# Kernel optimization log

Measured on AMD Instinct MI355X. Metric: run time of the kernel, lower is better.

Reference implementation:

```python
import jax, jax.numpy as jnp
import numpy as np

HUGE = jnp.float32(1e31)   # ops.HUGE_INT
EPS = 1e-20
B, AN = 1024, 256
D = 256            # emb_dim
HD = 512           # history_dim
AD = 2 * D         # action_dim
NE, NR = 100000, 400


def setup_inputs() -> dict:
    key = jax.random.key(0)
    ks = jax.random.split(key, 12)
    e = jax.random.randint(ks[0], (B,), 0, NE)
    q = jax.random.randint(ks[1], (B,), 0, NR)
    hstate = jax.random.normal(ks[2], (B, HD), dtype=jnp.float32)
    r_space = jax.random.randint(ks[3], (B, AN), 0, NR)
    e_space = jax.random.randint(ks[4], (B, AN), 0, NE)
    # binary action mask; guarantee at least one valid action per row
    action_mask = (jax.random.uniform(ks[5], (B, AN)) > 0.2).astype(jnp.float32)
    action_mask = action_mask.at[:, 0].set(1.0)
    entity_emb = jax.random.normal(ks[6], (NE, D), dtype=jnp.float32) * 0.02
    relation_emb = jax.random.normal(ks[7], (NR, D), dtype=jnp.float32) * 0.02
    W1 = jax.random.normal(ks[8], (2 * D + HD, AD), dtype=jnp.float32) * (1.0 / np.sqrt(2 * D + HD))
    b1 = jnp.zeros((AD,), dtype=jnp.float32)
    W2 = jax.random.normal(ks[9], (AD, AD), dtype=jnp.float32) * (1.0 / np.sqrt(AD))
    b2 = jnp.zeros((AD,), dtype=jnp.float32)
    return {"e": e, "q": q, "hstate": hstate, "r_space": r_space,
            "e_space": e_space, "action_mask": action_mask,
            "entity_emb": entity_emb, "relation_emb": relation_emb,
            "W1": W1, "b1": b1, "W2": W2, "b2": b2}


def reference(e, q, hstate, r_space, e_space, action_mask,
              entity_emb, relation_emb, W1, b1, W2, b2):
    Q = relation_emb[q]                       # [B, D]
    E = entity_emb[e]                         # [B, D]
    X = jnp.concatenate([E, hstate, Q], axis=-1)          # [B, 2D+HD]
    X = jax.nn.relu(X @ W1 + b1)                          # [B, AD]
    X2 = X @ W2 + b2                                      # [B, AD]
    # action embeddings: [rel_emb[r]; ent_emb[e]] per padded action slot
    A = jnp.concatenate([relation_emb[r_space], entity_emb[e_space]], axis=-1)  # [B, AN, AD]
    scores = jnp.einsum('bad,bd->ba', A, X2) - (1.0 - action_mask) * HUGE      # [B, AN]
    action_dist = jax.nn.softmax(scores, axis=-1)
    entropy = -jnp.sum(action_dist * jnp.log(jnp.clip(action_dist, EPS)), axis=-1)  # [B]
    return action_dist, entropy
```

## Files before the change

### kernel.cpp

```cpp
#include <hip/hip_runtime.h>
#include <math.h>

#define NB   1024
#define NACT 256
#define DIM  256
#define HDIM 512
#define ADIM 512
#define KTOT 1024
#define NE   100000
#define NR   400

typedef __attribute__((ext_vector_type(8))) short bf16x8;
typedef __attribute__((ext_vector_type(4))) float f32x4;

__device__ __forceinline__ unsigned short f2bf(float f) {
    unsigned int u = __float_as_uint(f);
    u += 0x7FFF + ((u >> 16) & 1);
    return (unsigned short)(u >> 16);
}
__device__ __forceinline__ float bf2f(unsigned short u) {
    return __uint_as_float(((unsigned int)u) << 16);
}

__global__ __launch_bounds__(256) void prep_stream(
    const float* __restrict__ ent, const float* __restrict__ rel,
    const float* __restrict__ hstate,
    const int* __restrict__ e, const int* __restrict__ q,
    ushort* __restrict__ entbf, ushort* __restrict__ relbf,
    ushort* __restrict__ Xbf)
{
    const int blk = blockIdx.x, tid = threadIdx.x;
    if (blk < 1024) {
        const float4* src = (const float4*)ent;
        ushort4* dst = (ushort4*)entbf;
        const int start = blk * 6250;
        for (int j = start + tid; j < start + 6250; j += 256) {
            const float4 v = src[j];
            ushort4 o = {f2bf(v.x), f2bf(v.y), f2bf(v.z), f2bf(v.w)};
            dst[j] = o;
        }
    } else if (blk < 1028) {
        const float4* src = (const float4*)rel;
        ushort4* dst = (ushort4*)relbf;
        const int start = (blk - 1024) * 6400;
        for (int j = start + tid; j < start + 6400; j += 256) {
            const float4 v = src[j];
            ushort4 o = {f2bf(v.x), f2bf(v.y), f2bf(v.z), f2bf(v.w)};
            dst[j] = o;
        }
    } else {
        const int b0 = (blk - 1028) * 16;
        const int c = tid * 4;
        for (int r = 0; r < 16; ++r) {
            const int b = b0 + r;
            float4 v;
            if (c < DIM)             v = *(const float4*)(ent + (size_t)e[b] * DIM + c);
            else if (c < DIM + HDIM) v = *(const float4*)(hstate + (size_t)b * HDIM + (c - DIM));
            else                     v = *(const float4*)(rel + (size_t)q[b] * DIM + (c - DIM - HDIM));
            ushort4 o = {f2bf(v.x), f2bf(v.y), f2bf(v.z), f2bf(v.w)};
            *(ushort4*)(Xbf + (size_t)b * KTOT + c) = o;
        }
    }
}

__global__ __launch_bounds__(256) void prep_transpose(
    const float* __restrict__ W1, const float* __restrict__ W2,
    ushort* __restrict__ W1T, ushort* __restrict__ W2T)
{
    __shared__ float t[64][68];
    const int z = blockIdx.z;
    if (z && blockIdx.x >= 8) return;
    const int Kd = z ? 512 : 1024;
    const float* in = z ? W2 : W1;
    ushort* out = z ? W2T : W1T;
    const int k0 = blockIdx.x * 64, n0 = blockIdx.y * 64;
    const int tid = threadIdx.x;
    const int kr = tid >> 2, c = tid & 3;
    #pragma unroll
    for (int j = 0; j < 4; ++j) {
        const float4 v = *(const float4*)(in + (size_t)(k0 + kr) * ADIM + n0 + c * 16 + j * 4);
        *(float4*)&t[kr][c * 16 + j * 4] = v;
    }
    __syncthreads();
    const int nr = tid >> 2;
    ushort tmp[16];
    #pragma unroll
    for (int kk = 0; kk < 16; ++kk) tmp[kk] = f2bf(t[c * 16 + kk][nr]);
    *(uint4*)(out + (size_t)(n0 + nr) * Kd + k0 + c * 16)     = *(uint4*)&tmp[0];
    *(uint4*)(out + (size_t)(n0 + nr) * Kd + k0 + c * 16 + 8) = *(uint4*)&tmp[8];
}

template<int K, bool RELU_BF16>
__global__ __launch_bounds__(256) void gemm_mfma(
    const ushort* __restrict__ A, const ushort* __restrict__ Bt,
    const float* __restrict__ bias, ushort* __restrict__ Cbf,
    float* __restrict__ Cf, int ldc)
{
    __shared__ __align__(16) ushort Als[64][40];
    __shared__ __align__(16) ushort Bls[64][40];
    const int tid  = threadIdx.x;
    const int n0   = blockIdx.x * 64;
    const int m0   = blockIdx.y * 64;
    const int wave = tid >> 6, lane = tid & 63;
    const int q    = lane >> 4, l15 = lane & 15;
    const int sm   = tid >> 2, sc = tid & 3;

    const uint4* ga = (const uint4*)(A  + (size_t)(m0 + sm) * K) + sc;
    const uint4* gb = (const uint4*)(Bt + (size_t)(n0 + sm) * K) + sc;

    f32x4 acc[4];
    #pragma unroll
    for (int mt = 0; mt < 4; ++mt) acc[mt] = (f32x4){0.f, 0.f, 0.f, 0.f};

    uint4 pa = ga[0], pb = gb[0];
    for (int it = 0; it < K / 32; ++it) {
        *(uint4*)&Als[sm][sc * 8] = pa;
        *(uint4*)&Bls[sm][sc * 8] = pb;
        __syncthreads();
        if (it + 1 < K / 32) {
            pa = ga[(it + 1) * 4];
            pb = gb[(it + 1) * 4];
        }
        const bf16x8 bfrag = *(const bf16x8*)&Bls[wave * 16 + l15][q * 8];
        #pragma unroll
        for (int mt = 0; mt < 4; ++mt) {
            const bf16x8 afrag = *(const bf16x8*)&Als[mt * 16 + l15][q * 8];
            acc[mt] = __builtin_amdgcn_mfma_f32_16x16x32_bf16(afrag, bfrag, acc[mt], 0, 0, 0);
        }
        __syncthreads();
    }
    const int n = n0 + wave * 16 + l15;
    const float bv = bias[n];
    #pragma unroll
    for (int mt = 0; mt < 4; ++mt) {
        #pragma unroll
        for (int r = 0; r < 4; ++r) {
            const int m = m0 + mt * 16 + q * 4 + r;
            const float v = acc[mt][r] + bv;
            if (RELU_BF16) Cbf[(size_t)m * ldc + n] = f2bf(fmaxf(v, 0.0f));
            else           Cf [(size_t)m * ldc + n] = v;
        }
    }
}

__global__ __launch_bounds__(512) void scores_kernel(
    const int* __restrict__ r_space, const int* __restrict__ e_space,
    const float* __restrict__ amask,
    const ushort* __restrict__ relbf, const ushort* __restrict__ entbf,
    const float* __restrict__ X2,
    float* __restrict__ dist_out, float* __restrict__ ent_out)
{
    const int b    = blockIdx.x;
    const int tid  = threadIdx.x;
    const int wave = tid >> 6;
    const int lane = tid & 63;

    __shared__ float xs[ADIM];
    __shared__ float sc[NACT];
    __shared__ int   ridx[NACT];
    __shared__ int   eidx[NACT];
    __shared__ float red1[8], red2[8], red3[8];

    if (tid < NACT) ridx[tid] = r_space[(size_t)b * NACT + tid];
    else            eidx[tid - NACT] = e_space[(size_t)b * NACT + tid - NACT];
    if (tid < ADIM / 4)
        ((float4*)xs)[tid] = ((const float4*)(X2 + (size_t)b * ADIM))[tid];
    __syncthreads();

    const float4 xr = ((const float4*)xs)[lane];
    const float4 xe = ((const float4*)(xs + DIM))[lane];

    const int abase = wave * 32;
    for (int a0 = abase; a0 < abase + 32; a0 += 8) {
        ushort4 rv[8], ev[8];
        #pragma unroll
        for (int i = 0; i < 8; ++i) {
            rv[i] = ((const ushort4*)relbf)[(size_t)ridx[a0 + i] * (DIM / 4) + lane];
            ev[i] = ((const ushort4*)entbf)[(size_t)eidx[a0 + i] * (DIM / 4) + lane];
        }
        float p[8];
        #pragma unroll
        for (int i = 0; i < 8; ++i) {
            p[i] = bf2f(rv[i].x) * xr.x + bf2f(rv[i].y) * xr.y
                 + bf2f(rv[i].z) * xr.z + bf2f(rv[i].w) * xr.w
                 + bf2f(ev[i].x) * xe.x + bf2f(ev[i].y) * xe.y
                 + bf2f(ev[i].z) * xe.z + bf2f(ev[i].w) * xe.w;
        }
        #pragma unroll
        for (int off = 32; off; off >>= 1) {
            #pragma unroll
            for (int i = 0; i < 8; ++i) p[i] += __shfl_xor(p[i], off);
        }
        float out = p[0];
        #pragma unroll
        for (int i = 1; i < 8; ++i) out = (lane == i) ? p[i] : out;
        if (lane < 8) sc[a0 + lane] = out;
    }
    __syncthreads();

    float s = -3.0e38f;
    if (tid < NACT) {
        const float m = amask[(size_t)b * NACT + tid];
        s = sc[tid] - (1.0f - m) * 1e31f;
    }

    float mx = s;
    #pragma unroll
    for (int off = 32; off; off >>= 1) mx = fmaxf(mx, __shfl_xor(mx, off));
    if (lane == 0) red1[wave] = mx;
    __syncthreads();
    mx = red1[0];
    #pragma unroll
    for (int w = 1; w < 8; ++w) mx = fmaxf(mx, red1[w]);

    const float ex = (tid < NACT) ? expf(s - mx) : 0.0f;
    float sum = ex;
    #pragma unroll
    for (int off = 32; off; off >>= 1) sum += __shfl_xor(sum, off);
    if (lane == 0) red2[wave] = sum;
    __syncthreads();
    sum = ((red2[0] + red2[1]) + (red2[2] + red2[3]))
        + ((red2[4] + red2[5]) + (red2[6] + red2[7]));

    const float d = ex / sum;
    if (tid < NACT) dist_out[(size_t)b * NACT + tid] = d;

    float t = (tid < NACT) ? d * logf(fmaxf(d, 1e-20f)) : 0.0f;
    #pragma unroll
    for (int off = 32; off; off >>= 1) t += __shfl_xor(t, off);
    if (lane == 0) red3[wave] = t;
    __syncthreads();
    if (tid == 0)
        ent_out[b] = -(((red3[0] + red3[1]) + (red3[2] + red3[3]))
                     + ((red3[4] + red3[5]) + (red3[6] + red3[7])));
}

extern "C" void kernel_launch(void* const* d_in, const int* in_sizes, int n_in,
                              void* d_out, int out_size, void* d_ws, size_t ws_size,
                              hipStream_t stream) {
    const int*   e       = (const int*)d_in[0];
    const int*   q       = (const int*)d_in[1];
    const float* hstate  = (const float*)d_in[2];
    const int*   r_space = (const int*)d_in[3];
    const int*   e_space = (const int*)d_in[4];
    const float* amask   = (const float*)d_in[5];
    const float* ent     = (const float*)d_in[6];
    const float* rel     = (const float*)d_in[7];
    const float* W1      = (const float*)d_in[8];
    const float* b1      = (const float*)d_in[9];
    const float* W2      = (const float*)d_in[10];
    const float* b2      = (const float*)d_in[11];

    ushort* Xbf   = (ushort*)d_ws;
    ushort* W1T   = Xbf   + (size_t)NB * KTOT;
    ushort* W2T   = W1T   + (size_t)ADIM * KTOT;
    ushort* Hbf   = W2T   + (size_t)ADIM * ADIM;
    ushort* entbf = Hbf   + (size_t)NB * ADIM;
    ushort* relbf = entbf + (size_t)NE * DIM;
    float*  X2    = (float*)(relbf + (size_t)NR * DIM);
    float*  dist  = (float*)d_out;
    float*  entr  = dist + (size_t)NB * NACT;

    prep_stream<<<1092, 256, 0, stream>>>(ent, rel, hstate, e, q, entbf, relbf, Xbf);
    prep_transpose<<<dim3(16, 8, 2), 256, 0, stream>>>(W1, W2, W1T, W2T);
    gemm_mfma<KTOT, true><<<dim3(ADIM / 64, NB / 64), 256, 0, stream>>>(
        Xbf, W1T, b1, Hbf, nullptr, ADIM);
    gemm_mfma<ADIM, false><<<dim3(ADIM / 64, NB / 64), 256, 0, stream>>>(
        Hbf, W2T, b2, nullptr, X2, ADIM);
    scores_kernel<<<NB, 512, 0, stream>>>(
        r_space, e_space, amask, relbf, entbf, X2, dist, entr);
}
```

Measured before the change: 234.7 us.

## Fuse embedding conversion with first GEMM, gathering fp32 rows inline

```diff
diff --git a/kernel.cpp b/kernel.cpp
--- a/kernel.cpp
+++ b/kernel.cpp
@@ -9,6 +9,7 @@
 #define KTOT 1024
 #define NE   100000
 #define NR   400
+#define CONVB 1024
 
 typedef __attribute__((ext_vector_type(8))) short bf16x8;
 typedef __attribute__((ext_vector_type(4))) float f32x4;
@@ -19,48 +20,7 @@
     return (unsigned short)(u >> 16);
 }
 __device__ __forceinline__ float bf2f(unsigned short u) {
-    return __uint_as_float(((unsigned int)u) << 16);
-}
-
-__global__ __launch_bounds__(256) void prep_stream(
-    const float* __restrict__ ent, const float* __restrict__ rel,
-    const float* __restrict__ hstate,
-    const int* __restrict__ e, const int* __restrict__ q,
-    ushort* __restrict__ entbf, ushort* __restrict__ relbf,
-    ushort* __restrict__ Xbf)
-{
-    const int blk = blockIdx.x, tid = threadIdx.x;
-    if (blk < 1024) {
-        const float4* src = (const float4*)ent;
-        ushort4* dst = (ushort4*)entbf;
-        const int start = blk * 6250;
-        for (int j = start + tid; j < start + 6250; j += 256) {
-            const float4 v = src[j];
-            ushort4 o = {f2bf(v.x), f2bf(v.y), f2bf(v.z), f2bf(v.w)};
-            dst[j] = o;
-        }
-    } else if (blk < 1028) {
-        const float4* src = (const float4*)rel;
-        ushort4* dst = (ushort4*)relbf;
-        const int start = (blk - 1024) * 6400;
-        for (int j = start + tid; j < start + 6400; j += 256) {
-            const float4 v = src[j];
-            ushort4 o = {f2bf(v.x), f2bf(v.y), f2bf(v.z), f2bf(v.w)};
-            dst[j] = o;
-        }
-    } else {
-        const int b0 = (blk - 1028) * 16;
-        const int c = tid * 4;
-        for (int r = 0; r < 16; ++r) {
-            const int b = b0 + r;
-            float4 v;
-            if (c < DIM)             v = *(const float4*)(ent + (size_t)e[b] * DIM + c);
-            else if (c < DIM + HDIM) v = *(const float4*)(hstate + (size_t)b * HDIM + (c - DIM));
-            else                     v = *(const float4*)(rel + (size_t)q[b] * DIM + (c - DIM - HDIM));
-            ushort4 o = {f2bf(v.x), f2bf(v.y), f2bf(v.z), f2bf(v.w)};
-            *(ushort4*)(Xbf + (size_t)b * KTOT + c) = o;
-        }
-    }
+    return __uint_as_float(((unsigned int)u) << 32 - 16);
 }
 
 __global__ __launch_bounds__(256) void prep_transpose(
@@ -90,11 +50,94 @@
     *(uint4*)(out + (size_t)(n0 + nr) * Kd + k0 + c * 16 + 8) = *(uint4*)&tmp[8];
 }
 
-template<int K, bool RELU_BF16>
-__global__ __launch_bounds__(256) void gemm_mfma(
+__global__ __launch_bounds__(256) void mega_conv_gemm1(
+    const float* __restrict__ ent, const float* __restrict__ rel,
+    const float* __restrict__ hstate,
+    const int* __restrict__ e, const int* __restrict__ q,
+    const ushort* __restrict__ W1T, const float* __restrict__ b1,
+    ushort* __restrict__ entbf, ushort* __restrict__ relbf,
+    ushort* __restrict__ Hbf)
+{
+    const int blk = blockIdx.x, tid = threadIdx.x;
+    __shared__ __align__(16) ushort Als[64][40];
+    __shared__ __align__(16) ushort Bls[64][40];
+
+    if (blk < CONVB) {
+        const float4* src = (const float4*)ent;
+        ushort4* dst = (ushort4*)entbf;
+        const int start = blk * 6250;
+        for (int j = start + tid; j < start + 6250; j += 256) {
+            const float4 v = src[j];
+            ushort4 o = {f2bf(v.x), f2bf(v.y), f2bf(v.z), f2bf(v.w)};
+            dst[j] = o;
+        }
+        if (blk < 100) {
+            const int j = blk * 256 + tid;
+            const float4 v = ((const float4*)rel)[j];
+            ushort4 o = {f2bf(v.x), f2bf(v.y), f2bf(v.z), f2bf(v.w)};
+            ((ushort4*)relbf)[j] = o;
+        }
+        return;
+    }
+
+    const int g  = blk - CONVB;
+    const int n0 = (g & 7) * 64;
+    const int m0 = (g >> 3) * 64;
+    const int wave = tid >> 6, lane = tid & 63;
+    const int qq   = lane >> 4, l15 = lane & 15;
+    const int sm   = tid >> 2, sc = tid & 3;
+    const int kofs = sc * 8;
+
+    const int row   = m0 + sm;
+    const float* rowE = ent + (size_t)e[row] * DIM;
+    const float* rowH = hstate + (size_t)row * HDIM - DIM;
+    const float* rowQ = rel + (size_t)q[row] * DIM - (DIM + HDIM);
+    const uint4* gb = (const uint4*)(W1T + (size_t)(n0 + sm) * KTOT) + sc;
+
+    f32x4 acc[4];
+    #pragma unroll
+    for (int mt = 0; mt < 4; ++mt) acc[mt] = (f32x4){0.f, 0.f, 0.f, 0.f};
+
+    float4 pa0 = *(const float4*)(rowE + kofs);
+    float4 pa1 = *(const float4*)(rowE + kofs + 4);
+    uint4  pb  = gb[0];
+
+    for (int it = 0; it < KTOT / 32; ++it) {
+        ushort t8[8];
+        t8[0] = f2bf(pa0.x); t8[1] = f2bf(pa0.y); t8[2] = f2bf(pa0.z); t8[3] = f2bf(pa0.w);
+        t8[4] = f2bf(pa1.x); t8[5] = f2bf(pa1.y); t8[6] = f2bf(pa1.z); t8[7] = f2bf(pa1.w);
+        *(uint4*)&Als[sm][sc * 8] = *(uint4*)t8;
+        *(uint4*)&Bls[sm][sc * 8] = pb;
+        __syncthreads();
+        if (it + 1 < KTOT / 32) {
+            const int kg = (it + 1) * 32 + kofs;
+            const float* src = (kg < DIM) ? rowE : ((kg < DIM + HDIM) ? rowH : rowQ);
+            pa0 = *(const float4*)(src + kg);
+            pa1 = *(const float4*)(src + kg + 4);
+            pb  = gb[(it + 1) * 4];
+        }
+        const bf16x8 bfrag = *(const bf16x8*)&Bls[wave * 16 + l15][qq * 8];
+        #pragma unroll
+        for (int mt = 0; mt < 4; ++mt) {
+            const bf16x8 afrag = *(const bf16x8*)&Als[mt * 16 + l15][qq * 8];
+            acc[mt] = __builtin_amdgcn_mfma_f32_16x16x32_bf16(afrag, bfrag, acc[mt], 0, 0, 0);
+        }
+        __syncthreads();
+    }
+    const int n = n0 + wave * 16 + l15;
+    const float bv = b1[n];
+    #pragma unroll
+    for (int mt = 0; mt < 4; ++mt)
+        #pragma unroll
+        for (int r = 0; r < 4; ++r) {
+            const int m = m0 + mt * 16 + qq * 4 + r;
+            Hbf[(size_t)m * ADIM + n] = f2bf(fmaxf(acc[mt][r] + bv, 0.0f));
+        }
+}
+
+__global__ __launch_bounds__(256) void gemm2_mfma(
     const ushort* __restrict__ A, const ushort* __restrict__ Bt,
-    const float* __restrict__ bias, ushort* __restrict__ Cbf,
-    float* __restrict__ Cf, int ldc)
+    const float* __restrict__ bias, float* __restrict__ Cf)
 {
     __shared__ __align__(16) ushort Als[64][40];
     __shared__ __align__(16) ushort Bls[64][40];
@@ -102,29 +145,29 @@
     const int n0   = blockIdx.x * 64;
     const int m0   = blockIdx.y * 64;
     const int wave = tid >> 6, lane = tid & 63;
-    const int q    = lane >> 4, l15 = lane & 15;
+    const int qq   = lane >> 4, l15 = lane & 15;
     const int sm   = tid >> 2, sc = tid & 3;
 
-    const uint4* ga = (const uint4*)(A  + (size_t)(m0 + sm) * K) + sc;
-    const uint4* gb = (const uint4*)(Bt + (size_t)(n0 + sm) * K) + sc;
+    const uint4* ga = (const uint4*)(A  + (size_t)(m0 + sm) * ADIM) + sc;
+    const uint4* gb = (const uint4*)(Bt + (size_t)(n0 + sm) * ADIM) + sc;
 
     f32x4 acc[4];
     #pragma unroll
     for (int mt = 0; mt < 4; ++mt) acc[mt] = (f32x4){0.f, 0.f, 0.f, 0.f};
 
     uint4 pa = ga[0], pb = gb[0];
-    for (int it = 0; it < K / 32; ++it) {
+    for (int it = 0; it < ADIM / 32; ++it) {
         *(uint4*)&Als[sm][sc * 8] = pa;
         *(uint4*)&Bls[sm][sc * 8] = pb;
         __syncthreads();
-        if (it + 1 < K / 32) {
+        if (it + 1 < ADIM / 32) {
             pa = ga[(it + 1) * 4];
             pb = gb[(it + 1) * 4];
         }
-        const bf16x8 bfrag = *(const bf16x8*)&Bls[wave * 16 + l15][q * 8];
+        const bf16x8 bfrag = *(const bf16x8*)&Bls[wave * 16 + l15][qq * 8];
         #pragma unroll
         for (int mt = 0; mt < 4; ++mt) {
-            const bf16x8 afrag = *(const bf16x8*)&Als[mt * 16 + l15][q * 8];
+            const bf16x8 afrag = *(const bf16x8*)&Als[mt * 16 + l15][qq * 8];
             acc[mt] = __builtin_amdgcn_mfma_f32_16x16x32_bf16(afrag, bfrag, acc[mt], 0, 0, 0);
         }
         __syncthreads();
@@ -132,15 +175,12 @@
     const int n = n0 + wave * 16 + l15;
     const float bv = bias[n];
     #pragma unroll
-    for (int mt = 0; mt < 4; ++mt) {
+    for (int mt = 0; mt < 4; ++mt)
         #pragma unroll
         for (int r = 0; r < 4; ++r) {
-            const int m = m0 + mt * 16 + q * 4 + r;
-            const float v = acc[mt][r] + bv;
-            if (RELU_BF16) Cbf[(size_t)m * ldc + n] = f2bf(fmaxf(v, 0.0f));
-            else           Cf [(size_t)m * ldc + n] = v;
-        }
-    }
+            const int m = m0 + mt * 16 + qq * 4 + r;
+            Cf[(size_t)m * ADIM + n] = acc[mt][r] + bv;
+        }
 }
 
 __global__ __launch_bounds__(512) void scores_kernel(
@@ -251,8 +291,7 @@
     const float* W2      = (const float*)d_in[10];
     const float* b2      = (const float*)d_in[11];
 
-    ushort* Xbf   = (ushort*)d_ws;
-    ushort* W1T   = Xbf   + (size_t)NB * KTOT;
+    ushort* W1T   = (ushort*)d_ws;
     ushort* W2T   = W1T   + (size_t)ADIM * KTOT;
     ushort* Hbf   = W2T   + (size_t)ADIM * ADIM;
     ushort* entbf = Hbf   + (size_t)NB * ADIM;
@@ -261,12 +300,10 @@
     float*  dist  = (float*)d_out;
     float*  entr  = dist + (size_t)NB * NACT;
 
-    prep_stream<<<1092, 256, 0, stream>>>(ent, rel, hstate, e, q, entbf, relbf, Xbf);
     prep_transpose<<<dim3(16, 8, 2), 256, 0, stream>>>(W1, W2, W1T, W2T);
-    gemm_mfma<KTOT, true><<<dim3(ADIM / 64, NB / 64), 256, 0, stream>>>(
-        Xbf, W1T, b1, Hbf, nullptr, ADIM);
-    gemm_mfma<ADIM, false><<<dim3(ADIM / 64, NB / 64), 256, 0, stream>>>(
-        Hbf, W2T, b2, nullptr, X2, ADIM);
+    mega_conv_gemm1<<<CONVB + 128, 256, 0, stream>>>(
+        ent, rel, hstate, e, q, W1T, b1, entbf, relbf, Hbf);
+    gemm2_mfma<<<dim3(ADIM / 64, NB / 64), 256, 0, stream>>>(Hbf, W2T, b2, X2);
     scores_kernel<<<NB, 512, 0, stream>>>(
         r_space, e_space, amask, relbf, entbf, X2, dist, entr);
 }
```

New measurement: 227.2 us. 3.2% less time.
